# Kernel optimization log

Hardware: AMD Instinct MI355X
Metric: run time of the kernel (lower is better)

Reference implementation:

```python
import jax, jax.numpy as jnp
import numpy as np
from jax import lax

DIM = 1024
B, N = 4, 4096


def setup_inputs() -> dict:
    key = jax.random.key(0)
    k1, k2 = jax.random.split(key)
    x = jax.random.normal(k1, (B, N, DIM), dtype=jnp.float32)
    # Linear(dim, 3*dim, bias=False): weight stored as [3*dim, dim] (torch convention)
    w_qkva = jax.random.normal(k2, (3 * DIM, DIM), dtype=jnp.float32) * (DIM ** -0.5)
    gamma = jnp.ones((DIM,), dtype=jnp.float32)  # RMSNorm gain
    return {"x": x, "w_qkva": w_qkva, "gamma": gamma}


def _rmsnorm(x, gamma):
    # lucidrains RMSNorm: F.normalize(x, dim=-1) * sqrt(dim) * gamma
    scale = jnp.asarray(x.shape[-1], x.dtype) ** 0.5
    norm = jnp.sqrt(jnp.sum(x * x, axis=-1, keepdims=True))
    return x / jnp.maximum(norm, 1e-12) * scale * gamma


def reference(x, w_qkva, gamma):
    h = _rmsnorm(x, gamma)                                  # [b, n, d]
    qkva = jnp.einsum('bnd,ed->bne', h, w_qkva)             # [b, n, 3d]
    q, kv, a = jnp.split(qkva, 3, axis=-1)                  # each [b, n, d]
    a = jax.nn.sigmoid(a)

    def binary_operator(e_i, e_j):
        a_i, kv_i = e_i
        a_j, kv_j = e_j
        return (a_j * a_i, a_j * kv_i + kv_j)

    # gated linear recurrence over the sequence axis (elementwise per channel)
    _, y = lax.associative_scan(binary_operator, (a, kv), axis=1)
    return q * y                                            # [b, n, d]
```

## Files before the change

### kernel.cpp

```cpp
#include <hip/hip_runtime.h>
#include <hip/hip_bf16.h>

#define SEQ_N 4096
#define BATCH 4
#define DIM 1024
#define M_ROWS (BATCH * SEQ_N)
#define NCOLS (3 * DIM)
#define KDIM DIM
#define CHUNK_L 16
#define NCHUNK (SEQ_N / CHUNK_L)
#define NCHANNEL (BATCH * DIM)
#define GT 32

using short8 = __attribute__((ext_vector_type(8))) short;
using f32x4  = __attribute__((ext_vector_type(4))) float;

static __device__ __forceinline__ unsigned short f2bf(float f) {
    union { float f; unsigned u; } v; v.f = f;
    unsigned r = v.u + 0x7fffu + ((v.u >> 16) & 1u);
    return (unsigned short)(r >> 16);
}
static __device__ __forceinline__ float bf2f(unsigned short s) {
    union { unsigned u; float f; } v; v.u = ((unsigned)s) << 16;
    return v.f;
}
static __device__ __forceinline__ float sigm(float x) {
    return 1.f / (1.f + __expf(-x));
}

#define WCONV_BLOCKS 3072
__global__ __launch_bounds__(256) void pre_kernel(const float* __restrict__ w,
                                                  unsigned short* __restrict__ wb,
                                                  const float* __restrict__ x,
                                                  const float* __restrict__ gamma,
                                                  unsigned short* __restrict__ h) {
    const int bid = blockIdx.x;
    const int tid = threadIdx.x;
    if (bid < WCONV_BLOCKS) {
        const int i = bid * 256 + tid;
        float4 v = reinterpret_cast<const float4*>(w)[i];
        ushort4 o;
        o.x = f2bf(v.x); o.y = f2bf(v.y); o.z = f2bf(v.z); o.w = f2bf(v.w);
        reinterpret_cast<ushort4*>(wb)[i] = o;
        return;
    }
    const int row = bid - WCONV_BLOCKS;
    const float4 v = reinterpret_cast<const float4*>(x + (size_t)row * DIM)[tid];
    float ss = v.x * v.x + v.y * v.y + v.z * v.z + v.w * v.w;
#pragma unroll
    for (int off = 32; off >= 1; off >>= 1) ss += __shfl_xor(ss, off, 64);
    __shared__ float red[4];
    if ((tid & 63) == 0) red[tid >> 6] = ss;
    __syncthreads();
    const float tot = red[0] + red[1] + red[2] + red[3];
    const float scale = 32.0f / fmaxf(sqrtf(tot), 1e-12f);
    const float4 g = reinterpret_cast<const float4*>(gamma)[tid];
    ushort4 o;
    o.x = f2bf(v.x * scale * g.x);
    o.y = f2bf(v.y * scale * g.y);
    o.z = f2bf(v.z * scale * g.z);
    o.w = f2bf(v.w * scale * g.w);
    reinterpret_cast<ushort4*>(h + (size_t)row * DIM)[tid] = o;
}

__global__ __launch_bounds__(512, 2) void gemm256_kernel(const unsigned short* __restrict__ A,
                                                         const unsigned short* __restrict__ B,
                                                         unsigned short* __restrict__ C) {
    __shared__ __align__(16) unsigned short sA[4][256][32];
    __shared__ __align__(16) unsigned short sB[4][256][32];

    const int tid  = threadIdx.x;
    const int lane = tid & 63;
    const int wave = tid >> 6;

    const int orig = blockIdx.x;
    const int xcd  = orig & 7;
    const int q    = orig >> 3;
    const int mtile = xcd * 8 + q / 12;
    const int ntile = q % 12;
    const int row0 = mtile * 256;
    const int col0 = ntile * 256;

    const int wm = (wave >> 2) * 128;
    const int wn = (wave & 3) * 64;
    const int fr = lane & 15;
    const int kq = lane >> 4;
    const int kqx = kq ^ ((fr >> 1) & 3);

    const int srow = tid >> 2;
    const int scol = ((tid & 3) ^ ((srow >> 1) & 3)) * 8;
    const unsigned short* aSrc = A + (size_t)(row0 + srow) * KDIM + scol;
    const unsigned short* bSrc = B + (size_t)(col0 + srow) * KDIM + scol;
    unsigned short* sAf = &sA[0][0][0];
    unsigned short* sBf = &sB[0][0][0];
    const int sdst = tid * 8;

#define STAGE_A(bs, kt, u)                                                              \
    __builtin_amdgcn_global_load_lds(                                                   \
        (const __attribute__((address_space(1))) void*)(aSrc + (size_t)(u) * 128 * KDIM + (kt) * 32), \
        (__attribute__((address_space(3))) void*)(sAf + (bs) * 8192 + (u) * 4096 + sdst), 16, 0, 0);
#define STAGE_B(bs, kt, u)                                                              \
    __builtin_amdgcn_global_load_lds(                                                   \
        (const __attribute__((address_space(1))) void*)(bSrc + (size_t)(u) * 128 * KDIM + (kt) * 32), \
        (__attribute__((address_space(3))) void*)(sBf + (bs) * 8192 + (u) * 4096 + sdst), 16, 0, 0);

    f32x4 acc[8][4] = {};

    STAGE_A(0, 0, 0); STAGE_A(0, 0, 1); STAGE_B(0, 0, 0); STAGE_B(0, 0, 1);
    STAGE_A(1, 1, 0); STAGE_A(1, 1, 1); STAGE_B(1, 1, 0); STAGE_B(1, 1, 1);
    asm volatile("s_waitcnt vmcnt(4)" ::: "memory");
    __builtin_amdgcn_sched_barrier(0);
    __builtin_amdgcn_s_barrier();

    for (int t = 0; t < GT; ++t) {
        const int b  = t & 3;
        const int bs = (t + 2) & 3;
        const bool st = (t + 2 < GT);
        const unsigned short* sAb = sAf + b * 8192;
        const unsigned short* sBb = sBf + b * 8192;

        short8 bfr[4], afr[4], afr2[4];
#pragma unroll
        for (int j = 0; j < 4; ++j)
            bfr[j] = *reinterpret_cast<const short8*>(sBb + (wn + j * 16 + fr) * 32 + kqx * 8);
#pragma unroll
        for (int i = 0; i < 4; ++i)
            afr[i] = *reinterpret_cast<const short8*>(sAb + (wm + i * 16 + fr) * 32 + kqx * 8);
#pragma unroll
        for (int i = 0; i < 4; ++i)
            afr2[i] = *reinterpret_cast<const short8*>(sAb + (wm + 64 + i * 16 + fr) * 32 + kqx * 8);

        if (st) { STAGE_A(bs, t + 2, 0); STAGE_A(bs, t + 2, 1);
                  STAGE_B(bs, t + 2, 0); STAGE_B(bs, t + 2, 1); }

        __builtin_amdgcn_s_setprio(1);
#pragma unroll
        for (int i = 0; i < 4; ++i)
#pragma unroll
            for (int j = 0; j < 4; ++j)
                acc[i][j] = __builtin_amdgcn_mfma_f32_16x16x32_bf16(afr[i], bfr[j], acc[i][j], 0, 0, 0);
#pragma unroll
        for (int i = 0; i < 4; ++i)
#pragma unroll
            for (int j = 0; j < 4; ++j)
                acc[4 + i][j] = __builtin_amdgcn_mfma_f32_16x16x32_bf16(afr2[i], bfr[j], acc[4 + i][j], 0, 0, 0);
        __builtin_amdgcn_s_setprio(0);

        if (t < GT - 2) {
            asm volatile("s_waitcnt vmcnt(4)" ::: "memory");
        } else if (t == GT - 2) {
            asm volatile("s_waitcnt vmcnt(0)" ::: "memory");
        }
        __builtin_amdgcn_sched_barrier(0);
        __builtin_amdgcn_s_barrier();
    }
#undef STAGE_A
#undef STAGE_B

#pragma unroll
    for (int i = 0; i < 8; ++i) {
#pragma unroll
        for (int j = 0; j < 4; ++j) {
#pragma unroll
            for (int r = 0; r < 4; ++r) {
                int row = row0 + wm + i * 16 + kq * 4 + r;
                int col = col0 + wn + j * 16 + fr;
                C[(size_t)row * NCOLS + col] = f2bf(acc[i][j][r]);
            }
        }
    }
}

__global__ __launch_bounds__(256) void chunk_agg_kernel(const unsigned short* __restrict__ qkva,
                                                        float* __restrict__ Aagg,
                                                        float* __restrict__ Yagg) {
    const int c = blockIdx.x, b = blockIdx.y;
    const int d4 = threadIdx.x * 4;
    const unsigned short* base = qkva + ((size_t)b * SEQ_N + c * CHUNK_L) * NCOLS;
    float s[4] = {0.f, 0.f, 0.f, 0.f};
    float A[4] = {1.f, 1.f, 1.f, 1.f};
#pragma unroll 4
    for (int n = 0; n < CHUNK_L; ++n) {
        const ushort4 kvu = *reinterpret_cast<const ushort4*>(base + (size_t)n * NCOLS + DIM + d4);
        const ushort4 au  = *reinterpret_cast<const ushort4*>(base + (size_t)n * NCOLS + 2 * DIM + d4);
        const float kv[4] = {bf2f(kvu.x), bf2f(kvu.y), bf2f(kvu.z), bf2f(kvu.w)};
        const float av[4] = {bf2f(au.x),  bf2f(au.y),  bf2f(au.z),  bf2f(au.w)};
#pragma unroll
        for (int j = 0; j < 4; ++j) {
            const float a = sigm(av[j]);
            s[j] = fmaf(a, s[j], kv[j]);
            A[j] *= a;
        }
    }
    const int idx = c * NCHANNEL + b * DIM + d4;
    float4 Ao, Yo;
    Ao.x = A[0]; Ao.y = A[1]; Ao.z = A[2]; Ao.w = A[3];
    Yo.x = s[0]; Yo.y = s[1]; Yo.z = s[2]; Yo.w = s[3];
    *reinterpret_cast<float4*>(&Aagg[idx]) = Ao;
    *reinterpret_cast<float4*>(&Yagg[idx]) = Yo;
}

__global__ __launch_bounds__(256) void agg_scan_kernel(const float* __restrict__ Aagg,
                                                       const float* __restrict__ Yagg,
                                                       float* __restrict__ Sin) {
    __shared__ float sA[NCHUNK][64];
    __shared__ float sY[NCHUNK][64];
    __shared__ float segA[4][64], segY[4][64];
    const int t = threadIdx.x;
    const int ch0 = blockIdx.x * 64;
    const int j = t & 63;
    const int g = t >> 6;
#pragma unroll 8
    for (int i = 0; i < 64; ++i) {
        const int c = i * 4 + g;
        sA[c][j] = Aagg[(size_t)c * NCHANNEL + ch0 + j];
        sY[c][j] = Yagg[(size_t)c * NCHANNEL + ch0 + j];
    }
    __syncthreads();
    float a = 1.f, y = 0.f;
#pragma unroll 8
    for (int i = 0; i < 64; ++i) {
        const int c = g * 64 + i;
        y = fmaf(sA[c][j], y, sY[c][j]);
        a *= sA[c][j];
    }
    segA[g][j] = a; segY[g][j] = y;
    __syncthreads();
    float s = 0.f;
#pragma unroll
    for (int gg = 0; gg < 3; ++gg)
        if (gg < g) s = fmaf(segA[gg][j], s, segY[gg][j]);
#pragma unroll 8
    for (int i = 0; i < 64; ++i) {
        const int c = g * 64 + i;
        Sin[(size_t)c * NCHANNEL + ch0 + j] = s;
        s = fmaf(sA[c][j], s, sY[c][j]);
    }
}

__global__ __launch_bounds__(256) void apply_kernel(const unsigned short* __restrict__ qkva,
                                                    const float* __restrict__ Sin,
                                                    float* __restrict__ out) {
    const int c = blockIdx.x, b = blockIdx.y;
    const int d4 = threadIdx.x * 4;
    const unsigned short* base = qkva + ((size_t)b * SEQ_N + c * CHUNK_L) * NCOLS;
    float* obase = out + ((size_t)b * SEQ_N + c * CHUNK_L) * DIM;
    const float4 s0 = *reinterpret_cast<const float4*>(&Sin[(size_t)c * NCHANNEL + b * DIM + d4]);
    float s[4] = {s0.x, s0.y, s0.z, s0.w};
#pragma unroll 4
    for (int n = 0; n < CHUNK_L; ++n) {
        const ushort4 qu  = *reinterpret_cast<const ushort4*>(base + (size_t)n * NCOLS + d4);
        const ushort4 kvu = *reinterpret_cast<const ushort4*>(base + (size_t)n * NCOLS + DIM + d4);
        const ushort4 au  = *reinterpret_cast<const ushort4*>(base + (size_t)n * NCOLS + 2 * DIM + d4);
        const float kv[4] = {bf2f(kvu.x), bf2f(kvu.y), bf2f(kvu.z), bf2f(kvu.w)};
        const float av[4] = {bf2f(au.x),  bf2f(au.y),  bf2f(au.z),  bf2f(au.w)};
        const float q[4]  = {bf2f(qu.x),  bf2f(qu.y),  bf2f(qu.z),  bf2f(qu.w)};
        float4 o;
#pragma unroll
        for (int j = 0; j < 4; ++j) {
            const float a = sigm(av[j]);
            s[j] = fmaf(a, s[j], kv[j]);
        }
        o.x = q[0] * s[0]; o.y = q[1] * s[1]; o.z = q[2] * s[2]; o.w = q[3] * s[3];
        *reinterpret_cast<float4*>(&obase[(size_t)n * DIM + d4]) = o;
    }
}

extern "C" void kernel_launch(void* const* d_in, const int* in_sizes, int n_in,
                              void* d_out, int out_size, void* d_ws, size_t ws_size,
                              hipStream_t stream) {
    const float* x     = (const float*)d_in[0];
    const float* w     = (const float*)d_in[1];
    const float* gamma = (const float*)d_in[2];
    float* out = (float*)d_out;

    char* ws = (char*)d_ws;
    unsigned short* wb   = (unsigned short*)(ws);
    unsigned short* h    = (unsigned short*)(ws + 6291456);
    unsigned short* qkva = (unsigned short*)(ws + 39845888);
    float* Aagg = (float*)(ws + 6291456);
    float* Yagg = (float*)(ws + 6291456 + 4194304);
    float* Sin  = (float*)(ws + 6291456 + 8388608);

    pre_kernel<<<WCONV_BLOCKS + M_ROWS, 256, 0, stream>>>(w, wb, x, gamma, h);
    gemm256_kernel<<<(M_ROWS / 256) * (NCOLS / 256), 512, 0, stream>>>(h, wb, qkva);
    chunk_agg_kernel<<<dim3(NCHUNK, BATCH), 256, 0, stream>>>(qkva, Aagg, Yagg);
    agg_scan_kernel<<<NCHANNEL / 64, 256, 0, stream>>>(Aagg, Yagg, Sin);
    apply_kernel<<<dim3(NCHUNK, BATCH), 256, 0, stream>>>(qkva, Sin, out);
}
```

Before: 273.8 us.

## Fuse chunk aggregation into GEMM epilogue with interleaved kv/a column tiles

Remaps GEMM N-tiles so each tile past the q section holds matching 128-column slices of kv and a. The epilogue stages the tile through LDS, then does coalesced 16-byte stores. When the workspace is large enough it also computes the per-chunk gated-scan aggregates directly from LDS, which removes the separate chunk_agg kernel and its re-read of kv and a. In exchange the epilogue gets extra LDS traffic, extra barriers and serial sigmoid work, and the fused path depends on the workspace size.

Result: slower. 313.1 us (+14.3%).

```diff
diff --git a/kernel.cpp b/kernel.cpp
--- a/kernel.cpp
+++ b/kernel.cpp
@@ -65,7 +65,9 @@
 
 __global__ __launch_bounds__(512, 2) void gemm256_kernel(const unsigned short* __restrict__ A,
                                                          const unsigned short* __restrict__ B,
-                                                         unsigned short* __restrict__ C) {
+                                                         unsigned short* __restrict__ C,
+                                                         float* __restrict__ Aagg,
+                                                         float* __restrict__ Yagg) {
     __shared__ __align__(16) unsigned short sA[4][256][32];
     __shared__ __align__(16) unsigned short sB[4][256][32];
 
@@ -79,7 +81,7 @@
     const int mtile = xcd * 8 + q / 12;
     const int ntile = q % 12;
     const int row0 = mtile * 256;
-    const int col0 = ntile * 256;
+    const int ds   = (ntile >= 4) ? (ntile - 4) * 128 : 0;
 
     const int wm = (wave >> 2) * 128;
     const int wn = (wave & 3) * 64;
@@ -90,7 +92,10 @@
     const int srow = tid >> 2;
     const int scol = ((tid & 3) ^ ((srow >> 1) & 3)) * 8;
     const unsigned short* aSrc = A + (size_t)(row0 + srow) * KDIM + scol;
-    const unsigned short* bSrc = B + (size_t)(col0 + srow) * KDIM + scol;
+    const int bRow0 = (ntile < 4) ? (ntile * 256 + srow)       : (1024 + ds + srow);
+    const int bRow1 = (ntile < 4) ? (ntile * 256 + 128 + srow) : (2048 + ds + srow);
+    const unsigned short* bSrc0 = B + (size_t)bRow0 * KDIM + scol;
+    const unsigned short* bSrc1 = B + (size_t)bRow1 * KDIM + scol;
     unsigned short* sAf = &sA[0][0][0];
     unsigned short* sBf = &sB[0][0][0];
     const int sdst = tid * 8;
@@ -101,7 +106,7 @@
         (__attribute__((address_space(3))) void*)(sAf + (bs) * 8192 + (u) * 4096 + sdst), 16, 0, 0);
 #define STAGE_B(bs, kt, u)                                                              \
     __builtin_amdgcn_global_load_lds(                                                   \
-        (const __attribute__((address_space(1))) void*)(bSrc + (size_t)(u) * 128 * KDIM + (kt) * 32), \
+        (const __attribute__((address_space(1))) void*)(((u) ? bSrc1 : bSrc0) + (kt) * 32), \
         (__attribute__((address_space(3))) void*)(sBf + (bs) * 8192 + (u) * 4096 + sdst), 16, 0, 0);
 
     f32x4 acc[8][4] = {};
@@ -157,17 +162,68 @@
 #undef STAGE_A
 #undef STAGE_B
 
-#pragma unroll
-    for (int i = 0; i < 8; ++i) {
-#pragma unroll
-        for (int j = 0; j < 4; ++j) {
-#pragma unroll
-            for (int r = 0; r < 4; ++r) {
-                int row = row0 + wm + i * 16 + kq * 4 + r;
-                int col = col0 + wn + j * 16 + fr;
-                C[(size_t)row * NCOLS + col] = f2bf(acc[i][j][r]);
+    unsigned short* sE = sAf;
+    const int doAgg = (Aagg != nullptr) && (ntile >= 4);
+#pragma unroll 1
+    for (int half = 0; half < 2; ++half) {
+        if ((wave >> 2) == half) {
+#pragma unroll
+            for (int i = 0; i < 8; ++i) {
+#pragma unroll
+                for (int j = 0; j < 4; ++j) {
+#pragma unroll
+                    for (int r = 0; r < 4; ++r) {
+                        const int lrow = i * 16 + kq * 4 + r;
+                        const int col  = wn + j * 16 + fr;
+                        const int g    = col >> 3;
+                        sE[lrow * 256 + ((g ^ (lrow & 7)) * 8) + (col & 7)] =
+                            f2bf(acc[i][j][r]);
+                    }
+                }
             }
         }
+        __syncthreads();
+        {
+            const int lrow = tid >> 2;
+            const int gb   = tid & 3;
+            const size_t rowbase = (size_t)(row0 + half * 128 + lrow) * NCOLS;
+#pragma unroll
+            for (int s = 0; s < 8; ++s) {
+                const int g = gb + s * 4;
+                const short8 v = *reinterpret_cast<const short8*>(
+                    sE + lrow * 256 + ((g ^ (lrow & 7)) * 8));
+                const int gcol = (ntile < 4) ? (ntile * 256 + g * 8)
+                               : ((g < 16) ? (1024 + ds + g * 8)
+                                           : (2048 + ds + (g - 16) * 8));
+                *reinterpret_cast<short8*>(&C[rowbase + gcol]) = v;
+            }
+        }
+        if (doAgg) {
+#pragma unroll 1
+            for (int rd = 0; rd < 2; ++rd) {
+                const int item = tid + rd * 512;
+                const int ck   = item >> 7;
+                const int ch   = item & 127;
+                float s = 0.f, P = 1.f;
+#pragma unroll
+                for (int i = 0; i < 16; ++i) {
+                    const int lr = ck * 16 + i;
+                    const int gk = (ch >> 3) ^ (lr & 7);
+                    const int ga = ((ch >> 3) + 16) ^ (lr & 7);
+                    const float kv = bf2f(sE[lr * 256 + gk * 8 + (ch & 7)]);
+                    const float av = bf2f(sE[lr * 256 + ga * 8 + (ch & 7)]);
+                    const float a  = sigm(av);
+                    s = fmaf(a, s, kv);
+                    P *= a;
+                }
+                const int cg = ((row0 & (SEQ_N - 1)) >> 4) + half * 8 + ck;
+                const int bb = row0 >> 12;
+                const size_t ai = (size_t)cg * NCHANNEL + (size_t)bb * DIM + ds + ch;
+                Aagg[ai] = P;
+                Yagg[ai] = s;
+            }
+        }
+        __syncthreads();
     }
 }
 
@@ -278,13 +334,24 @@
     unsigned short* wb   = (unsigned short*)(ws);
     unsigned short* h    = (unsigned short*)(ws + 6291456);
     unsigned short* qkva = (unsigned short*)(ws + 39845888);
-    float* Aagg = (float*)(ws + 6291456);
-    float* Yagg = (float*)(ws + 6291456 + 4194304);
-    float* Sin  = (float*)(ws + 6291456 + 8388608);
+
+    const bool fused = (ws_size >= 148897792);
+    float *Aagg, *Yagg, *Sin;
+    if (fused) {
+        Aagg = (float*)(ws + 140509184);
+        Yagg = (float*)(ws + 140509184 + 4194304);
+        Sin  = (float*)(ws + 6291456);
+    } else {
+        Aagg = (float*)(ws + 6291456);
+        Yagg = (float*)(ws + 6291456 + 4194304);
+        Sin  = (float*)(ws + 6291456 + 8388608);
+    }
 
     pre_kernel<<<WCONV_BLOCKS + M_ROWS, 256, 0, stream>>>(w, wb, x, gamma, h);
-    gemm256_kernel<<<(M_ROWS / 256) * (NCOLS / 256), 512, 0, stream>>>(h, wb, qkva);
-    chunk_agg_kernel<<<dim3(NCHUNK, BATCH), 256, 0, stream>>>(qkva, Aagg, Yagg);
+    gemm256_kernel<<<(M_ROWS / 256) * (NCOLS / 256), 512, 0, stream>>>(
+        h, wb, qkva, fused ? Aagg : nullptr, fused ? Yagg : nullptr);
+    if (!fused)
+        chunk_agg_kernel<<<dim3(NCHUNK, BATCH), 256, 0, stream>>>(qkva, Aagg, Yagg);
     agg_scan_kernel<<<NCHANNEL / 64, 256, 0, stream>>>(Aagg, Yagg, Sin);
     apply_kernel<<<dim3(NCHUNK, BATCH), 256, 0, stream>>>(qkva, Sin, out);
 }
```
